# Kernel optimization log

Hardware: AMD Instinct MI355X
Metric: run time of the kernel (lower is better)

The kernel has to match this reference:

```python
import jax, jax.numpy as jnp
import numpy as np

B, N, F, H = 8, 256, 512, 256  # batch, nodes (=hidden_dim), feature_dim, hidden_dim


def _pair_scores(x, y, W1a, W1b, b1, W2, b2):
    """sigmoid(MLP(concat(x_i, y_j))) for all pairs, without materializing concat.

    x, y: [B, N, H]. W1a/W1b are the two halves of the Linear(2H -> H) weight.
    Returns [B, N, N].
    """
    a = jnp.einsum('bnh,hk->bnk', x, W1a)          # contribution of row i
    c = jnp.einsum('bnh,hk->bnk', y, W1b)          # contribution of row j
    h = jax.nn.relu(a[:, :, None, :] + c[:, None, :, :] + b1)  # [B,N,N,H]
    s = jnp.einsum('bijh,h->bij', h, W2) + b2
    return jax.nn.sigmoid(s)


def setup_inputs() -> dict:
    key = jax.random.key(0)
    ks = jax.random.split(key, 16)
    sc = 0.02
    return {
        'image_features': jax.random.normal(ks[0], (B, N, F), jnp.float32),
        'text_features': jax.random.normal(ks[1], (B, N, F), jnp.float32),
        # feature_transform: Linear(F->H), ReLU, Linear(H->H)
        'ft_W1': jax.random.normal(ks[2], (F, H), jnp.float32) * sc,
        'ft_b1': jnp.zeros((H,), jnp.float32),
        'ft_W2': jax.random.normal(ks[3], (H, H), jnp.float32) * sc,
        'ft_b2': jnp.zeros((H,), jnp.float32),
        # structure_learning: Linear(2H->H) split into two H x H halves, Linear(H->1)
        'sl_W1a': jax.random.normal(ks[4], (H, H), jnp.float32) * sc,
        'sl_W1b': jax.random.normal(ks[5], (H, H), jnp.float32) * sc,
        'sl_b1': jnp.zeros((H,), jnp.float32),
        'sl_W2': jax.random.normal(ks[6], (H,), jnp.float32) * sc,
        'sl_b2': jnp.zeros((), jnp.float32),
        # causal_net: Linear(2H->H) split, Linear(H->1)
        'cn_W1a': jax.random.normal(ks[7], (H, H), jnp.float32) * sc,
        'cn_W1b': jax.random.normal(ks[8], (H, H), jnp.float32) * sc,
        'cn_b1': jnp.zeros((H,), jnp.float32),
        'cn_W2': jax.random.normal(ks[9], (H,), jnp.float32) * sc,
        'cn_b2': jnp.zeros((), jnp.float32),
    }


def reference(image_features, text_features,
              ft_W1, ft_b1, ft_W2, ft_b2,
              sl_W1a, sl_W1b, sl_b1, sl_W2, sl_b2,
              cn_W1a, cn_W1b, cn_b1, cn_W2, cn_b2):
    # --- StructuralLearning ---
    def feat(x):
        h = jax.nn.relu(jnp.einsum('bnf,fh->bnh', x, ft_W1) + ft_b1)
        return jnp.einsum('bnh,hk->bnk', h, ft_W2) + ft_b2

    img_h = feat(image_features)   # [B,N,H]
    txt_h = feat(text_features)    # [B,N,H]
    structure = _pair_scores(img_h, txt_h, sl_W1a, sl_W1b, sl_b1, sl_W2, sl_b2)  # [B,N,N]

    # --- CausalDiscovery (batched over all node pairs; sigmoid(structure) > 0
    # everywhere so every (i,j) is an edge). DAG cycle removal is a CPU-side
    # networkx post-process and is omitted from the differentiable reference. ---
    causal_matrix = _pair_scores(structure, structure, cn_W1a, cn_W1b, cn_b1, cn_W2, cn_b2)

    # --- verify_causal_invariance ---
    stability = jnp.mean(jnp.abs(causal_matrix - jnp.roll(causal_matrix, 1, axis=0)))
    consistency = jnp.mean(jnp.std(causal_matrix, axis=0, ddof=1))  # torch.std is unbiased
    invariance_score = 1.0 - (stability + consistency) / 2

    return structure, causal_matrix, invariance_score
```

## Files before the change

### kernel.cpp

```cpp
#include <hip/hip_runtime.h>
#include <math.h>

#define B_ 8
#define N_ 256
#define F_ 512
#define H_ 256

typedef __attribute__((ext_vector_type(8))) short short8;
typedef __attribute__((ext_vector_type(4))) float floatx4;

__device__ __forceinline__ unsigned int f2bf_bits(float f) {
    unsigned int u = __float_as_uint(f);
    return (u + 0x7fffu + ((u >> 16) & 1u)) >> 16;
}
__device__ __forceinline__ unsigned int pack2bf(float a, float b) {
    return f2bf_bits(a) | (f2bf_bits(b) << 16);
}
__device__ __forceinline__ float bf_lo(unsigned int u) { return __uint_as_float(u << 16); }
__device__ __forceinline__ float bf_hi(unsigned int u) { return __uint_as_float(u & 0xffff0000u); }

__global__ __launch_bounds__(256) void prep_weights(
    const float* __restrict__ ftW1, const float* __restrict__ ftW2,
    const float* __restrict__ slW1a, const float* __restrict__ slW1b,
    const float* __restrict__ cnW1a, const float* __restrict__ cnW1b,
    unsigned short* __restrict__ wt)
{
    int t = blockIdx.x * 256 + threadIdx.x;
    const float* src; int K; unsigned short* dst;
    if (t < 16384) { src = ftW1; K = 512; dst = wt; }
    else {
        int m  = (t - 16384) >> 13;
        int lt = (t - 16384) & 8191;
        t = lt; K = 256;
        switch (m) {
            case 0:  src = ftW2;  dst = wt + 131072; break;
            case 1:  src = slW1a; dst = wt + 196608; break;
            case 2:  src = slW1b; dst = wt + 262144; break;
            case 3:  src = cnW1a; dst = wt + 327680; break;
            default: src = cnW1b; dst = wt + 393216; break;
        }
    }
    const int n  = t & 255;
    const int k0 = (t >> 8) * 8;
    unsigned int p[4];
#pragma unroll
    for (int j = 0; j < 4; ++j) {
        float f0 = src[(size_t)(k0 + 2 * j)     * 256 + n];
        float f1 = src[(size_t)(k0 + 2 * j + 1) * 256 + n];
        p[j] = pack2bf(f0, f1);
    }
    *(uint4*)(dst + (size_t)n * K + k0) = make_uint4(p[0], p[1], p[2], p[3]);
}

__global__ __launch_bounds__(256) void gemm_mfma(
    const void* __restrict__ A0, const void* __restrict__ A1, int aSplitBlk, int aBf16,
    const unsigned short* __restrict__ Wt0, const unsigned short* __restrict__ Wt1,
    const float* __restrict__ bias0, const float* __restrict__ bias1,
    int wRowSplitBlk, int wColSplitBlk,
    void* __restrict__ out, int outBf16, int ldOut, int K, int relu)
{
    __shared__ unsigned short As[64][40];
    __shared__ unsigned short Bs[64][40];

    const int tid = threadIdx.x;
    const int bx = blockIdx.x, by = blockIdx.y;

    const void* Abase; int arow0;
    if (by < aSplitBlk) { Abase = A0; arow0 = by * 64; }
    else                { Abase = A1; arow0 = (by - aSplitBlk) * 64; }

    int wcolBlk = bx;
    bool second;
    if (wColSplitBlk > 0) {
        second = (bx >= wColSplitBlk);
        if (second) wcolBlk = bx - wColSplitBlk;
    } else {
        second = (by >= wRowSplitBlk);
    }
    const unsigned short* Wt = second ? Wt1 : Wt0;
    const float* bias        = second ? bias1 : bias0;
    const int wcol = wcolBlk * 64;

    const int r    = tid >> 2;
    const int kq   = (tid & 3) * 8;
    const int lane = tid & 63;
    const int wv   = tid >> 6;
    const int col  = lane & 15;
    const int quad = lane >> 4;

    floatx4 acc[4] = {};

    uint4 apack, bpack;
    float4 af0, af1;
    const unsigned short* Abf = (const unsigned short*)Abase + (size_t)(arow0 + r) * K + kq;
    const float*          Afp = (const float*)Abase + (size_t)(arow0 + r) * K + kq;
    const unsigned short* Wp  = Wt + (size_t)(wcol + r) * K + kq;

    if (aBf16) apack = *(const uint4*)(Abf);
    else { af0 = *(const float4*)(Afp); af1 = *(const float4*)(Afp + 4); }
    bpack = *(const uint4*)(Wp);

    for (int k0 = 0; k0 < K; k0 += 32) {
        uint4 aw;
        if (aBf16) aw = apack;
        else aw = make_uint4(pack2bf(af0.x, af0.y), pack2bf(af0.z, af0.w),
                             pack2bf(af1.x, af1.y), pack2bf(af1.z, af1.w));
        uint4 bw = bpack;

        __syncthreads();
        *(uint4*)&As[r][kq] = aw;
        *(uint4*)&Bs[r][kq] = bw;
        __syncthreads();

        if (k0 + 32 < K) {
            if (aBf16) apack = *(const uint4*)(Abf + k0 + 32);
            else {
                af0 = *(const float4*)(Afp + k0 + 32);
                af1 = *(const float4*)(Afp + k0 + 32 + 4);
            }
            bpack = *(const uint4*)(Wp + k0 + 32);
        }

        short8 bfrag = *(const short8*)&Bs[wv * 16 + col][quad * 8];
#pragma unroll
        for (int tm = 0; tm < 4; ++tm) {
            short8 afrag = *(const short8*)&As[tm * 16 + col][quad * 8];
            acc[tm] = __builtin_amdgcn_mfma_f32_16x16x32_bf16(afrag, bfrag, acc[tm], 0, 0, 0);
        }
    }

    const int ocol = bx * 64 + wv * 16 + col;
    const int bcol = wcol + wv * 16 + col;
    const float bv = bias ? bias[bcol] : 0.f;
#pragma unroll
    for (int tm = 0; tm < 4; ++tm) {
#pragma unroll
        for (int rr = 0; rr < 4; ++rr) {
            float v = acc[tm][rr] + bv;
            if (relu) v = fmaxf(v, 0.f);
            const size_t o = (size_t)(by * 64 + tm * 16 + quad * 4 + rr) * ldOut + ocol;
            if (outBf16) ((unsigned short*)out)[o] = (unsigned short)f2bf_bits(v);
            else         ((float*)out)[o] = v;
        }
    }
}

__global__ __launch_bounds__(256) void pair_score(
    const unsigned short* __restrict__ Abase, int ldA,
    const unsigned short* __restrict__ Cbase, int ldC,
    const float* __restrict__ W2, const float* __restrict__ b2p,
    float* __restrict__ out)
{
    __shared__ unsigned short aS[32][256];
    __shared__ unsigned short cS[32][256];
    __shared__ float w2S[H_];

    const int tid = threadIdx.x;
    const int b   = blockIdx.z;
    const int i0b = blockIdx.y * 32;
    const int j0b = blockIdx.x * 32;

    {
        const int r   = tid >> 3;
        const int c8  = tid & 7;
        const int key = (r >> 1) & 7;
        const unsigned short* Ar = Abase + ((size_t)b * N_ + i0b + r) * ldA;
        const unsigned short* Cr = Cbase + ((size_t)b * N_ + j0b + r) * ldC;
#pragma unroll
        for (int rep = 0; rep < 4; ++rep) {
            const int ch = c8 + rep * 8;
            uint4 va = *(const uint4*)(Ar + ch * 8);
            uint4 vc = *(const uint4*)(Cr + ch * 8);
            const int pc = (ch ^ key) << 3;
            *(uint4*)&aS[r][pc] = va;
            *(uint4*)&cS[r][pc] = vc;
        }
        w2S[tid] = W2[tid];
    }
    __syncthreads();

    const int ti = tid >> 4, tj = tid & 15;
    const int ia = ti * 2, jc = tj * 2;
    const int keyA = ti & 7, keyC = tj & 7;

    float s00 = 0.f, s01 = 0.f, s10 = 0.f, s11 = 0.f;
#pragma unroll 4
    for (int h = 0; h < H_; h += 4) {
        const int chunk = h >> 3, sub = h & 7;
        const int pa = ((chunk ^ keyA) << 3) | sub;
        const int pc = ((chunk ^ keyC) << 3) | sub;
        uint2 ua0 = *(const uint2*)&aS[ia][pa];
        uint2 ua1 = *(const uint2*)&aS[ia + 1][pa];
        uint2 uc0 = *(const uint2*)&cS[jc][pc];
        uint2 uc1 = *(const uint2*)&cS[jc + 1][pc];
        float4 w  = *(const float4*)&w2S[h];
        float a0[4] = { bf_lo(ua0.x), bf_hi(ua0.x), bf_lo(ua0.y), bf_hi(ua0.y) };
        float a1[4] = { bf_lo(ua1.x), bf_hi(ua1.x), bf_lo(ua1.y), bf_hi(ua1.y) };
        float c0[4] = { bf_lo(uc0.x), bf_hi(uc0.x), bf_lo(uc0.y), bf_hi(uc0.y) };
        float c1[4] = { bf_lo(uc1.x), bf_hi(uc1.x), bf_lo(uc1.y), bf_hi(uc1.y) };
        float wv[4] = { w.x, w.y, w.z, w.w };
#pragma unroll
        for (int q = 0; q < 4; ++q) {
            s00 = fmaf(fmaxf(a0[q] + c0[q], 0.f), wv[q], s00);
            s01 = fmaf(fmaxf(a0[q] + c1[q], 0.f), wv[q], s01);
            s10 = fmaf(fmaxf(a1[q] + c0[q], 0.f), wv[q], s10);
            s11 = fmaf(fmaxf(a1[q] + c1[q], 0.f), wv[q], s11);
        }
    }
    const float bb = b2p[0];
    const size_t ob = ((size_t)b * N_ + i0b + ia) * N_ + j0b + jc;
    out[ob]           = 1.f / (1.f + expf(-(s00 + bb)));
    out[ob + 1]       = 1.f / (1.f + expf(-(s01 + bb)));
    out[ob + N_]      = 1.f / (1.f + expf(-(s10 + bb)));
    out[ob + N_ + 1]  = 1.f / (1.f + expf(-(s11 + bb)));
}

__global__ __launch_bounds__(256) void invariance_partial(
    const float* __restrict__ causal, float* __restrict__ accum)
{
    const int idx = blockIdx.x * 256 + threadIdx.x;
    float x[B_];
#pragma unroll
    for (int b = 0; b < B_; ++b) x[b] = causal[(size_t)b * (N_ * N_) + idx];

    float stab = 0.f, mean = 0.f;
#pragma unroll
    for (int b = 0; b < B_; ++b) {
        stab += fabsf(x[b] - x[(b + B_ - 1) % B_]);
        mean += x[b];
    }
    mean *= (1.f / B_);
    float var = 0.f;
#pragma unroll
    for (int b = 0; b < B_; ++b) {
        float d = x[b] - mean;
        var = fmaf(d, d, var);
    }
    float sd = sqrtf(var * (1.f / (B_ - 1)));

#pragma unroll
    for (int off = 32; off > 0; off >>= 1) {
        stab += __shfl_down(stab, off, 64);
        sd   += __shfl_down(sd, off, 64);
    }
    if ((threadIdx.x & 63) == 0) {
        atomicAdd(&accum[0], stab);
        atomicAdd(&accum[1], sd);
    }
}

__global__ void finalize_kernel(const float* __restrict__ accum,
                                float* __restrict__ out_scalar)
{
    float stability   = accum[0] * (1.f / (float)(B_ * N_ * N_));
    float consistency = accum[1] * (1.f / (float)(N_ * N_));
    out_scalar[0] = 1.f - (stability + consistency) * 0.5f;
}

extern "C" void kernel_launch(void* const* d_in, const int* in_sizes, int n_in,
                              void* d_out, int out_size, void* d_ws, size_t ws_size,
                              hipStream_t stream)
{
    const float* img   = (const float*)d_in[0];
    const float* txt   = (const float*)d_in[1];
    const float* ftW1  = (const float*)d_in[2];
    const float* ftb1  = (const float*)d_in[3];
    const float* ftW2  = (const float*)d_in[4];
    const float* ftb2  = (const float*)d_in[5];
    const float* slW1a = (const float*)d_in[6];
    const float* slW1b = (const float*)d_in[7];
    const float* slb1  = (const float*)d_in[8];
    const float* slW2  = (const float*)d_in[9];
    const float* slb2  = (const float*)d_in[10];
    const float* cnW1a = (const float*)d_in[11];
    const float* cnW1b = (const float*)d_in[12];
    const float* cnb1  = (const float*)d_in[13];
    const float* cnW2  = (const float*)d_in[14];
    const float* cnb2  = (const float*)d_in[15];

    float* out       = (float*)d_out;
    float* structure = out;
    float* causal    = out + (size_t)B_ * N_ * N_;
    float* inv       = out + 2 * (size_t)B_ * N_ * N_;

    unsigned short* wt   = (unsigned short*)d_ws;
    unsigned short* h1b  = wt + 524288;
    unsigned short* h12b = h1b + 1048576;
    unsigned short* acb  = h12b + 1048576;
    unsigned short* ac2b = acb + 1048576;
    float* accum         = (float*)(ac2b + 1048576);

    hipMemsetAsync(accum, 0, 2 * sizeof(float), stream);

    dim3 blk(256);
    const int BIG = 1 << 20;

    prep_weights<<<dim3(224), blk, 0, stream>>>(ftW1, ftW2, slW1a, slW1b, cnW1a, cnW1b, wt);

    const unsigned short* wtFT1 = wt;
    const unsigned short* wtFT2 = wt + 131072;
    const unsigned short* wtSLA = wt + 196608;
    const unsigned short* wtSLB = wt + 262144;
    const unsigned short* wtCNA = wt + 327680;
    const unsigned short* wtCNB = wt + 393216;

    gemm_mfma<<<dim3(4, 64), blk, 0, stream>>>(
        img, txt, 32, 0, wtFT1, wtFT1, ftb1, ftb1, BIG, 0,
        h1b, 1, 256, 512, 1);
    gemm_mfma<<<dim3(4, 64), blk, 0, stream>>>(
        h1b, h1b, BIG, 1, wtFT2, wtFT2, ftb2, ftb2, BIG, 0,
        h12b, 1, 256, 256, 0);
    gemm_mfma<<<dim3(4, 64), blk, 0, stream>>>(
        h12b, h12b, BIG, 1, wtSLA, wtSLB, nullptr, slb1, 32, 0,
        acb, 1, 256, 256, 0);
    pair_score<<<dim3(8, 8, 8), blk, 0, stream>>>(
        acb, 256, acb + (size_t)2048 * 256, 256, slW2, slb2, structure);
    gemm_mfma<<<dim3(8, 32), blk, 0, stream>>>(
        structure, structure, BIG, 0, wtCNA, wtCNB, nullptr, cnb1, BIG, 4,
        ac2b, 1, 512, 256, 0);
    pair_score<<<dim3(8, 8, 8), blk, 0, stream>>>(
        ac2b, 512, ac2b + 256, 512, cnW2, cnb2, causal);
    invariance_partial<<<dim3(N_ * N_ / 256), blk, 0, stream>>>(causal, accum);
    finalize_kernel<<<dim3(1), dim3(1), 0, stream>>>(accum, inv);
}
```

Before: 191.6 us.

## Fold ftW2 into structure weights, fp32 pair intermediates, double-buffer GEMM LDS

Precomputes the products ftW2·slW1a and ftW2·slW1b, plus the matching folded biases, so one GEMM replaces two in the feature and structure path. The pair_score intermediates change from bf16 to fp32, which doubles their memory traffic and LDS footprint but removes the bf16 unpacking. The GEMM moves to double-buffered LDS with one barrier per k-step. The finalize kernel is merged into invariance_partial using a last-block atomic counter.

After: 176.9 us. -7.7%, faster.

```diff
diff --git a/kernel.cpp b/kernel.cpp
--- a/kernel.cpp
+++ b/kernel.cpp
@@ -16,40 +16,67 @@
 __device__ __forceinline__ unsigned int pack2bf(float a, float b) {
     return f2bf_bits(a) | (f2bf_bits(b) << 16);
 }
-__device__ __forceinline__ float bf_lo(unsigned int u) { return __uint_as_float(u << 16); }
-__device__ __forceinline__ float bf_hi(unsigned int u) { return __uint_as_float(u & 0xffff0000u); }
 
 __global__ __launch_bounds__(256) void prep_weights(
     const float* __restrict__ ftW1, const float* __restrict__ ftW2,
     const float* __restrict__ slW1a, const float* __restrict__ slW1b,
     const float* __restrict__ cnW1a, const float* __restrict__ cnW1b,
-    unsigned short* __restrict__ wt)
-{
+    const float* __restrict__ ftb2, const float* __restrict__ slb1,
+    unsigned short* __restrict__ wt, float* __restrict__ bA, float* __restrict__ bB)
+{
+    if (blockIdx.x >= 224) {
+        const int second = (blockIdx.x == 225);
+        const float* W = second ? slW1b : slW1a;
+        const int n = threadIdx.x;
+        float s0 = 0.f, s1 = 0.f, s2 = 0.f, s3 = 0.f;
+#pragma unroll 4
+        for (int k = 0; k < 256; k += 4) {
+            s0 = fmaf(ftb2[k],     W[(k)     * 256 + n], s0);
+            s1 = fmaf(ftb2[k + 1], W[(k + 1) * 256 + n], s1);
+            s2 = fmaf(ftb2[k + 2], W[(k + 2) * 256 + n], s2);
+            s3 = fmaf(ftb2[k + 3], W[(k + 3) * 256 + n], s3);
+        }
+        float s = (s0 + s1) + (s2 + s3);
+        if (second) bB[n] = s + slb1[n];
+        else        bA[n] = s;
+        return;
+    }
+
     int t = blockIdx.x * 256 + threadIdx.x;
-    const float* src; int K; unsigned short* dst;
-    if (t < 16384) { src = ftW1; K = 512; dst = wt; }
-    else {
-        int m  = (t - 16384) >> 13;
-        int lt = (t - 16384) & 8191;
-        t = lt; K = 256;
-        switch (m) {
-            case 0:  src = ftW2;  dst = wt + 131072; break;
-            case 1:  src = slW1a; dst = wt + 196608; break;
-            case 2:  src = slW1b; dst = wt + 262144; break;
-            case 3:  src = cnW1a; dst = wt + 327680; break;
-            default: src = cnW1b; dst = wt + 393216; break;
-        }
-    }
-    const int n  = t & 255;
-    const int k0 = (t >> 8) * 8;
-    unsigned int p[4];
-#pragma unroll
-    for (int j = 0; j < 4; ++j) {
-        float f0 = src[(size_t)(k0 + 2 * j)     * 256 + n];
-        float f1 = src[(size_t)(k0 + 2 * j + 1) * 256 + n];
-        p[j] = pack2bf(f0, f1);
-    }
-    *(uint4*)(dst + (size_t)n * K + k0) = make_uint4(p[0], p[1], p[2], p[3]);
+    if (t < 49152) {
+        const float* src; int K; unsigned short* dst;
+        if (t < 16384) { src = ftW1; K = 512; dst = wt; }
+        else {
+            int m  = (t - 16384) >> 13;
+            t = (t - 16384) & 8191; K = 256;
+            switch (m) {
+                case 0:  src = slW1a; dst = wt + 131072; break;
+                case 1:  src = slW1b; dst = wt + 196608; break;
+                case 2:  src = cnW1a; dst = wt + 262144; break;
+                default: src = cnW1b; dst = wt + 327680; break;
+            }
+        }
+        const int n  = t & 255;
+        const int k0 = (t >> 8) * 8;
+        unsigned int p[4];
+#pragma unroll
+        for (int j = 0; j < 4; ++j) {
+            float f0 = src[(size_t)(k0 + 2 * j)     * 256 + n];
+            float f1 = src[(size_t)(k0 + 2 * j + 1) * 256 + n];
+            p[j] = pack2bf(f0, f1);
+        }
+        *(uint4*)(dst + (size_t)n * K + k0) = make_uint4(p[0], p[1], p[2], p[3]);
+    } else {
+        const int lt = t - 49152;
+        const int k  = lt >> 5;
+        const int n0 = (lt & 31) * 8;
+        const float* src = ftW2 + (size_t)k * 256 + n0;
+        float4 f0 = *(const float4*)(src);
+        float4 f1 = *(const float4*)(src + 4);
+        unsigned short* dst = wt + 393216 + (size_t)k * 256 + n0;
+        *(uint4*)dst = make_uint4(pack2bf(f0.x, f0.y), pack2bf(f0.z, f0.w),
+                                  pack2bf(f1.x, f1.y), pack2bf(f1.z, f1.w));
+    }
 }
 
 __global__ __launch_bounds__(256) void gemm_mfma(
@@ -59,8 +86,8 @@
     int wRowSplitBlk, int wColSplitBlk,
     void* __restrict__ out, int outBf16, int ldOut, int K, int relu)
 {
-    __shared__ unsigned short As[64][40];
-    __shared__ unsigned short Bs[64][40];
+    __shared__ unsigned short As[2][64][40];
+    __shared__ unsigned short Bs[2][64][40];
 
     const int tid = threadIdx.x;
     const int bx = blockIdx.x, by = blockIdx.y;
@@ -100,6 +127,7 @@
     else { af0 = *(const float4*)(Afp); af1 = *(const float4*)(Afp + 4); }
     bpack = *(const uint4*)(Wp);
 
+    int p = 0;
     for (int k0 = 0; k0 < K; k0 += 32) {
         uint4 aw;
         if (aBf16) aw = apack;
@@ -107,10 +135,8 @@
                              pack2bf(af1.x, af1.y), pack2bf(af1.z, af1.w));
         uint4 bw = bpack;
 
-        __syncthreads();
-        *(uint4*)&As[r][kq] = aw;
-        *(uint4*)&Bs[r][kq] = bw;
-        __syncthreads();
+        *(uint4*)&As[p][r][kq] = aw;
+        *(uint4*)&Bs[p][r][kq] = bw;
 
         if (k0 + 32 < K) {
             if (aBf16) apack = *(const uint4*)(Abf + k0 + 32);
@@ -121,12 +147,15 @@
             bpack = *(const uint4*)(Wp + k0 + 32);
         }
 
-        short8 bfrag = *(const short8*)&Bs[wv * 16 + col][quad * 8];
+        __syncthreads();
+
+        short8 bfrag = *(const short8*)&Bs[p][wv * 16 + col][quad * 8];
 #pragma unroll
         for (int tm = 0; tm < 4; ++tm) {
-            short8 afrag = *(const short8*)&As[tm * 16 + col][quad * 8];
+            short8 afrag = *(const short8*)&As[p][tm * 16 + col][quad * 8];
             acc[tm] = __builtin_amdgcn_mfma_f32_16x16x32_bf16(afrag, bfrag, acc[tm], 0, 0, 0);
         }
+        p ^= 1;
     }
 
     const int ocol = bx * 64 + wv * 16 + col;
@@ -146,14 +175,13 @@
 }
 
 __global__ __launch_bounds__(256) void pair_score(
-    const unsigned short* __restrict__ Abase, int ldA,
-    const unsigned short* __restrict__ Cbase, int ldC,
+    const float* __restrict__ Abase, int ldA,
+    const float* __restrict__ Cbase, int ldC,
     const float* __restrict__ W2, const float* __restrict__ b2p,
     float* __restrict__ out)
 {
-    __shared__ unsigned short aS[32][256];
-    __shared__ unsigned short cS[32][256];
-    __shared__ float w2S[H_];
+    __shared__ float aS[32][256];
+    __shared__ float cS[32][256];
 
     const int tid = threadIdx.x;
     const int b   = blockIdx.z;
@@ -164,18 +192,17 @@
         const int r   = tid >> 3;
         const int c8  = tid & 7;
         const int key = (r >> 1) & 7;
-        const unsigned short* Ar = Abase + ((size_t)b * N_ + i0b + r) * ldA;
-        const unsigned short* Cr = Cbase + ((size_t)b * N_ + j0b + r) * ldC;
-#pragma unroll
-        for (int rep = 0; rep < 4; ++rep) {
+        const float* Ar = Abase + ((size_t)b * N_ + i0b + r) * ldA;
+        const float* Cr = Cbase + ((size_t)b * N_ + j0b + r) * ldC;
+#pragma unroll
+        for (int rep = 0; rep < 8; ++rep) {
             const int ch = c8 + rep * 8;
-            uint4 va = *(const uint4*)(Ar + ch * 8);
-            uint4 vc = *(const uint4*)(Cr + ch * 8);
-            const int pc = (ch ^ key) << 3;
-            *(uint4*)&aS[r][pc] = va;
-            *(uint4*)&cS[r][pc] = vc;
-        }
-        w2S[tid] = W2[tid];
+            float4 va = *(const float4*)(Ar + ch * 4);
+            float4 vc = *(const float4*)(Cr + ch * 4);
+            const int pc = (ch ^ key) << 2;
+            *(float4*)&aS[r][pc] = va;
+            *(float4*)&cS[r][pc] = vc;
+        }
     }
     __syncthreads();
 
@@ -186,25 +213,25 @@
     float s00 = 0.f, s01 = 0.f, s10 = 0.f, s11 = 0.f;
 #pragma unroll 4
     for (int h = 0; h < H_; h += 4) {
-        const int chunk = h >> 3, sub = h & 7;
-        const int pa = ((chunk ^ keyA) << 3) | sub;
-        const int pc = ((chunk ^ keyC) << 3) | sub;
-        uint2 ua0 = *(const uint2*)&aS[ia][pa];
-        uint2 ua1 = *(const uint2*)&aS[ia + 1][pa];
-        uint2 uc0 = *(const uint2*)&cS[jc][pc];
-        uint2 uc1 = *(const uint2*)&cS[jc + 1][pc];
-        float4 w  = *(const float4*)&w2S[h];
-        float a0[4] = { bf_lo(ua0.x), bf_hi(ua0.x), bf_lo(ua0.y), bf_hi(ua0.y) };
-        float a1[4] = { bf_lo(ua1.x), bf_hi(ua1.x), bf_lo(ua1.y), bf_hi(ua1.y) };
-        float c0[4] = { bf_lo(uc0.x), bf_hi(uc0.x), bf_lo(uc0.y), bf_hi(uc0.y) };
-        float c1[4] = { bf_lo(uc1.x), bf_hi(uc1.x), bf_lo(uc1.y), bf_hi(uc1.y) };
-        float wv[4] = { w.x, w.y, w.z, w.w };
+        const int chunk = h >> 2;
+        const int pa = (chunk ^ keyA) << 2;
+        const int pc = (chunk ^ keyC) << 2;
+        float4 a0 = *(const float4*)&aS[ia][pa];
+        float4 a1 = *(const float4*)&aS[ia + 1][pa];
+        float4 c0 = *(const float4*)&cS[jc][pc];
+        float4 c1 = *(const float4*)&cS[jc + 1][pc];
+        float4 w  = *(const float4*)&W2[h];
+        float av0[4] = { a0.x, a0.y, a0.z, a0.w };
+        float av1[4] = { a1.x, a1.y, a1.z, a1.w };
+        float cv0[4] = { c0.x, c0.y, c0.z, c0.w };
+        float cv1[4] = { c1.x, c1.y, c1.z, c1.w };
+        float wv[4]  = { w.x,  w.y,  w.z,  w.w  };
 #pragma unroll
         for (int q = 0; q < 4; ++q) {
-            s00 = fmaf(fmaxf(a0[q] + c0[q], 0.f), wv[q], s00);
-            s01 = fmaf(fmaxf(a0[q] + c1[q], 0.f), wv[q], s01);
-            s10 = fmaf(fmaxf(a1[q] + c0[q], 0.f), wv[q], s10);
-            s11 = fmaf(fmaxf(a1[q] + c1[q], 0.f), wv[q], s11);
+            s00 = fmaf(fmaxf(av0[q] + cv0[q], 0.f), wv[q], s00);
+            s01 = fmaf(fmaxf(av0[q] + cv1[q], 0.f), wv[q], s01);
+            s10 = fmaf(fmaxf(av1[q] + cv0[q], 0.f), wv[q], s10);
+            s11 = fmaf(fmaxf(av1[q] + cv1[q], 0.f), wv[q], s11);
         }
     }
     const float bb = b2p[0];
@@ -216,7 +243,8 @@
 }
 
 __global__ __launch_bounds__(256) void invariance_partial(
-    const float* __restrict__ causal, float* __restrict__ accum)
+    const float* __restrict__ causal, float* __restrict__ accum,
+    float* __restrict__ out_scalar)
 {
     const int idx = blockIdx.x * 256 + threadIdx.x;
     float x[B_];
@@ -243,18 +271,28 @@
         stab += __shfl_down(stab, off, 64);
         sd   += __shfl_down(sd, off, 64);
     }
+
+    __shared__ float red[8];
     if ((threadIdx.x & 63) == 0) {
-        atomicAdd(&accum[0], stab);
-        atomicAdd(&accum[1], sd);
-    }
-}
-
-__global__ void finalize_kernel(const float* __restrict__ accum,
-                                float* __restrict__ out_scalar)
-{
-    float stability   = accum[0] * (1.f / (float)(B_ * N_ * N_));
-    float consistency = accum[1] * (1.f / (float)(N_ * N_));
-    out_scalar[0] = 1.f - (stability + consistency) * 0.5f;
+        red[threadIdx.x >> 6]     = stab;
+        red[4 + (threadIdx.x >> 6)] = sd;
+    }
+    __syncthreads();
+    if (threadIdx.x == 0) {
+        float s = (red[0] + red[1]) + (red[2] + red[3]);
+        float d = (red[4] + red[5]) + (red[6] + red[7]);
+        atomicAdd(&accum[0], s);
+        atomicAdd(&accum[1], d);
+        __threadfence();
+        unsigned int prev = atomicAdd((unsigned int*)&accum[2], 1u);
+        if (prev == 255u) {
+            float st  = atomicAdd(&accum[0], 0.f);
+            float sdt = atomicAdd(&accum[1], 0.f);
+            float stability   = st  * (1.f / (float)(B_ * N_ * N_));
+            float consistency = sdt * (1.f / (float)(N_ * N_));
+            out_scalar[0] = 1.f - (stability + consistency) * 0.5f;
+        }
+    }
 }
 
 extern "C" void kernel_launch(void* const* d_in, const int* in_sizes, int n_in,
@@ -283,43 +321,51 @@
     float* causal    = out + (size_t)B_ * N_ * N_;
     float* inv       = out + 2 * (size_t)B_ * N_ * N_;
 
-    unsigned short* wt   = (unsigned short*)d_ws;
-    unsigned short* h1b  = wt + 524288;
-    unsigned short* h12b = h1b + 1048576;
-    unsigned short* acb  = h12b + 1048576;
-    unsigned short* ac2b = acb + 1048576;
-    float* accum         = (float*)(ac2b + 1048576);
-
-    hipMemsetAsync(accum, 0, 2 * sizeof(float), stream);
+    unsigned short* wt     = (unsigned short*)d_ws;
+    unsigned short* wcombT = wt + 458752;
+    float* bA    = (float*)(wt + 589824);
+    float* bB    = bA + 256;
+    float* accum = bA + 512;
+    unsigned short* h1b = wt + 655360;
+    float* acb   = (float*)(wt + 1703936);
+    float* ac2b  = acb;
+
+    hipMemsetAsync(accum, 0, 4 * sizeof(float), stream);
 
     dim3 blk(256);
     const int BIG = 1 << 20;
 
-    prep_weights<<<dim3(224), blk, 0, stream>>>(ftW1, ftW2, slW1a, slW1b, cnW1a, cnW1b, wt);
-
     const unsigned short* wtFT1 = wt;
-    const unsigned short* wtFT2 = wt + 131072;
-    const unsigned short* wtSLA = wt + 196608;
-    const unsigned short* wtSLB = wt + 262144;
-    const unsigned short* wtCNA = wt + 327680;
-    const unsigned short* wtCNB = wt + 393216;
+    const unsigned short* wtSLA = wt + 131072;
+    const unsigned short* wtSLB = wt + 196608;
+    const unsigned short* wtCNA = wt + 262144;
+    const unsigned short* wtCNB = wt + 327680;
+    const unsigned short* ftW2r = wt + 393216;
+
+    prep_weights<<<dim3(226), blk, 0, stream>>>(
+        ftW1, ftW2, slW1a, slW1b, cnW1a, cnW1b, ftb2, slb1, wt, bA, bB);
+
+    gemm_mfma<<<dim3(4, 8), blk, 0, stream>>>(
+        wtSLA, wtSLB, 4, 1, ftW2r, ftW2r, nullptr, nullptr, BIG, 0,
+        wcombT, 1, 256, 256, 0);
 
     gemm_mfma<<<dim3(4, 64), blk, 0, stream>>>(
         img, txt, 32, 0, wtFT1, wtFT1, ftb1, ftb1, BIG, 0,
         h1b, 1, 256, 512, 1);
+
     gemm_mfma<<<dim3(4, 64), blk, 0, stream>>>(
-        h1b, h1b, BIG, 1, wtFT2, wtFT2, ftb2, ftb2, BIG, 0,
-        h12b, 1, 256, 256, 0);
-    gemm_mfma<<<dim3(4, 64), blk, 0, stream>>>(
-        h12b, h12b, BIG, 1, wtSLA, wtSLB, nullptr, slb1, 32, 0,
-        acb, 1, 256, 256, 0);
+        h1b, h1b, BIG, 1, wcombT, wcombT + 65536, bA, bB, 32, 0,
+        acb, 0, 256, 256, 0);
+
     pair_score<<<dim3(8, 8, 8), blk, 0, stream>>>(
         acb, 256, acb + (size_t)2048 * 256, 256, slW2, slb2, structure);
+
     gemm_mfma<<<dim3(8, 32), blk, 0, stream>>>(
         structure, structure, BIG, 0, wtCNA, wtCNB, nullptr, cnb1, BIG, 4,
-        ac2b, 1, 512, 256, 0);
+        ac2b, 0, 512, 256, 0);
+
     pair_score<<<dim3(8, 8, 8), blk, 0, stream>>>(
         ac2b, 512, ac2b + 256, 512, cnW2, cnb2, causal);
-    invariance_partial<<<dim3(N_ * N_ / 256), blk, 0, stream>>>(causal, accum);
-    finalize_kernel<<<dim3(1), dim3(1), 0, stream>>>(accum, inv);
-}
+
+    invariance_partial<<<dim3(N_ * N_ / 256), blk, 0, stream>>>(causal, accum, inv);
+}
```
